# Kernel optimization log

Measured on AMD Instinct MI355X. Metric: run time of the kernel, lower is better.

Reference implementation:

```python
import jax, jax.numpy as jnp
import numpy as np

IN_DIM, HID, MEM, OUT = 512, 1024, 1024, 512
BATCH = 4096
HIST = 5  # hist_steps hard-coded in MMU.__init__

_LINEARS = [("inpgate", IN_DIM, HID), ("rec_inpgate", OUT, HID), ("mem_inpgate", MEM, HID),
            ("inp", IN_DIM, HID), ("rec_inp", OUT, HID),
            ("readgate", IN_DIM, MEM), ("rec_readgate", OUT, MEM), ("mem_readgate", MEM, MEM),
            ("decoder", HID, MEM),
            ("writegate", IN_DIM, MEM), ("rec_writegate", OUT, MEM), ("mem_writegate", MEM, MEM),
            ("encoder", MEM, HID)]


def setup_inputs() -> dict:
    key = jax.random.key(0)
    ks = iter(jax.random.split(key, 2 * len(_LINEARS) + 4))
    d = {"input": jax.random.normal(next(ks), (IN_DIM, BATCH), jnp.float32)}
    for name, fin, fout in _LINEARS:
        bound = 1.0 / np.sqrt(fin)  # torch nn.Linear default init range
        d["W_" + name] = jax.random.uniform(next(ks), (fout, fin), jnp.float32, -bound, bound)
        d["b_" + name] = jax.random.uniform(next(ks), (fout,), jnp.float32, -bound, bound)
    d["w_hid_out"] = jax.random.uniform(next(ks), (OUT, MEM), jnp.float32)  # torch.rand
    return d


def reference(input, W_inpgate, b_inpgate, W_rec_inpgate, b_rec_inpgate,
              W_mem_inpgate, b_mem_inpgate, W_inp, b_inp, W_rec_inp, b_rec_inp,
              W_readgate, b_readgate, W_rec_readgate, b_rec_readgate,
              W_mem_readgate, b_mem_readgate, W_decoder, b_decoder,
              W_writegate, b_writegate, W_rec_writegate, b_rec_writegate,
              W_mem_writegate, b_mem_writegate, W_encoder, b_encoder, w_hid_out):
    B = input.shape[1]
    lin = lambda x, W, b: x @ W.T + b
    # fresh module: history is zeros except last slot = current input (transposed to [B, in])
    xs = jnp.concatenate([jnp.zeros((HIST - 1, B, IN_DIM), input.dtype), input.T[None]], axis=0)

    def step(carry, x):
        out, mem = carry  # [B, OUT], [B, MEM]
        block_inp = jax.nn.sigmoid(lin(x, W_inp, b_inp) + lin(out, W_rec_inp, b_rec_inp))
        inp_gate = jax.nn.sigmoid(lin(x, W_inpgate, b_inpgate) + lin(mem, W_mem_inpgate, b_mem_inpgate)
                                  + lin(out, W_rec_inpgate, b_rec_inpgate))
        read_gate = jax.nn.sigmoid(lin(x, W_readgate, b_readgate) + lin(mem, W_mem_readgate, b_mem_readgate)
                                   + lin(out, W_rec_readgate, b_rec_readgate))
        decoded_mem = lin(read_gate * mem, W_decoder, b_decoder)
        hidden = decoded_mem + block_inp * inp_gate  # [B, HID] (HID == MEM)
        write_gate = jax.nn.sigmoid(lin(x, W_writegate, b_writegate) + lin(mem, W_mem_writegate, b_mem_writegate)
                                    + lin(out, W_rec_writegate, b_rec_writegate))
        encoded = jnp.tanh(lin(hidden, W_encoder, b_encoder))
        mem = (1.0 - write_gate) * mem + write_gate * encoded
        out = hidden @ w_hid_out.T  # w_hid_out.mm(hidden.T).T
        return (out, mem), None

    init = (jnp.zeros((B, OUT), input.dtype), jnp.zeros((B, MEM), input.dtype))
    (out, _mem), _ = jax.lax.scan(step, init, xs)
    return out
```

## Files before the change

### kernel.cpp

```cpp
#include <hip/hip_runtime.h>
#include <hip/hip_bf16.h>
#include <math.h>

typedef __hip_bfloat16 bf16;
typedef __attribute__((ext_vector_type(8))) short s16x8;
typedef __attribute__((ext_vector_type(4))) float f32x4;

__device__ __forceinline__ float fsig(float x) {
  return __builtin_amdgcn_rcpf(1.0f + __expf(-x));
}
__device__ __forceinline__ float ftanh(float x) { return 2.0f * fsig(2.0f * x) - 1.0f; }
__device__ __forceinline__ float dot4(float4 a, float4 b) {
  return a.x * b.x + a.y * b.y + a.z * b.z + a.w * b.w;
}
__device__ __forceinline__ float wred(float s) {
#pragma unroll
  for (int off = 32; off > 0; off >>= 1) s += __shfl_down(s, off, 64);
  return s;
}
__device__ __forceinline__ float b2f(unsigned short u) {
  return __uint_as_float((unsigned)u << 16);
}
__device__ __forceinline__ float4 b2f4(ushort4 u) {
  return make_float4(b2f(u.x), b2f(u.y), b2f(u.z), b2f(u.w));
}

#define WG7_STRIDE 5120

__global__ void setup(const float* __restrict__ W_inp, const float* __restrict__ W_ig,
                      const float* __restrict__ W_rg, const float* __restrict__ W_ho,
                      const float* __restrict__ W_dec, const float* __restrict__ W_enc,
                      const float* __restrict__ input,
                      const float* __restrict__ Wri, const float* __restrict__ Wmig,
                      const float* __restrict__ Wrig, const float* __restrict__ Wmrg,
                      const float* __restrict__ Wrrg, const float* __restrict__ Wmwg,
                      const float* __restrict__ Wrwg,
                      const float* __restrict__ b_inp, const float* __restrict__ b_rinp,
                      const float* __restrict__ b_ig, const float* __restrict__ b_mig,
                      const float* __restrict__ b_rig, const float* __restrict__ b_wg,
                      const float* __restrict__ b_mwg, const float* __restrict__ b_rwg,
                      const float* __restrict__ b_dec, const float* __restrict__ b_enc,
                      bf16* __restrict__ Wcat,
                      bf16* __restrict__ WhoB, bf16* __restrict__ Wcat2, bf16* __restrict__ Wdt,
                      bf16* __restrict__ WencB, bf16* __restrict__ Xb,
                      float* __restrict__ out_s, float* __restrict__ mem_s,
                      float* __restrict__ vout, float* __restrict__ Web,
                      bf16* __restrict__ Wg7) {
  __shared__ float t[32][33];
  const int id = blockIdx.x, tid = threadIdx.x;
  if (id < 12288) {
    const int i = id * 256 + tid;
    if (i < 524288) {
      Wcat[i] = __float2bfloat16(W_inp[i]);
    } else if (i < 1048576) {
      Wcat[i] = __float2bfloat16(W_ig[i - 524288]);
    } else if (i < 1572864) {
      Wcat[i] = __float2bfloat16(W_rg[i - 1048576]);
    } else if (i < 2097152) {
      const int k = i - 1572864;
      const bf16 vv = __float2bfloat16(W_ho[k]);
      WhoB[k] = vv;
      Wcat2[(size_t)(k >> 10) * 2048 + (k & 1023)] = vv;
    } else {
      const int k = i - 2097152;
      WencB[k] = __float2bfloat16(W_enc[k]);
    }
  } else if (id < 14336) {
    const int b = id - 12288;
    const int i0 = (b >> 7) * 32, b0 = (b & 127) * 32;
    const int tx = tid & 31, ty = tid >> 5;
#pragma unroll
    for (int r = ty; r < 32; r += 8) t[r][tx] = input[(size_t)(i0 + r) * 4096 + b0 + tx];
    __syncthreads();
#pragma unroll
    for (int r = ty; r < 32; r += 8)
      Xb[(size_t)(b0 + r) * 512 + i0 + tx] = __float2bfloat16(t[tx][r]);
  } else if (id < 15360) {
    const int b = id - 14336;
    const int j0 = (b >> 5) * 32, k0 = (b & 31) * 32;
    const int tx = tid & 31, ty = tid >> 5;
#pragma unroll
    for (int r = ty; r < 32; r += 8) t[r][tx] = W_dec[(size_t)(j0 + r) * 1024 + k0 + tx];
    __syncthreads();
#pragma unroll
    for (int r = ty; r < 32; r += 8)
      Wdt[(size_t)(k0 + r) * 1024 + j0 + tx] = __float2bfloat16(t[tx][r]);
  } else if (id < 16896) {
    const int o = id - 15360;
    const float* row = (o < 512) ? (W_ho + (size_t)o * 1024) : (W_enc + (size_t)(o - 512) * 1024);
    const float4 a = *(const float4*)(row + tid * 4);
    const float4 b = *(const float4*)(b_dec + tid * 4);
    float s = wred(dot4(a, b));
    if ((tid & 63) == 0) t[0][tid >> 6] = s;
    __syncthreads();
    if (tid == 0) {
      const float d = t[0][0] + t[0][1] + t[0][2] + t[0][3];
      if (o < 512) vout[o] = d;
      else Web[o - 512] = d;
    }
  } else if (id < 18432) {
    const int id2 = id - 16896;
    const float4 bd = *(const float4*)(b_dec + tid * 4);
    const float4 v1 = *(const float4*)(b_inp + tid * 4);
    const float4 v2 = *(const float4*)(b_rinp + tid * 4);
    const float4 v3 = *(const float4*)(b_ig + tid * 4);
    const float4 v4 = *(const float4*)(b_mig + tid * 4);
    const float4 v5 = *(const float4*)(b_rig + tid * 4);
    float4 hv;
    hv.x = bd.x + fsig(v1.x + v2.x) * fsig(v3.x + v4.x + v5.x);
    hv.y = bd.y + fsig(v1.y + v2.y) * fsig(v3.y + v4.y + v5.y);
    hv.z = bd.z + fsig(v1.z + v2.z) * fsig(v3.z + v4.z + v5.z);
    hv.w = bd.w + fsig(v1.w + v2.w) * fsig(v3.w + v4.w + v5.w);
    const float* row =
        (id2 < 1024) ? (W_enc + (size_t)id2 * 1024) : (W_ho + (size_t)(id2 - 1024) * 1024);
    float s = wred(dot4(*(const float4*)(row + tid * 4), hv));
    if ((tid & 63) == 0) t[0][tid >> 6] = s;
    __syncthreads();
    if (tid == 0) {
      const float d = t[0][0] + t[0][1] + t[0][2] + t[0][3];
      if (id2 < 1024) {
        const float wg = fsig(b_wg[id2] + b_mwg[id2] + b_rwg[id2]);
        mem_s[id2] = wg * ftanh(b_enc[id2] + d);
      } else {
        out_s[id2 - 1024] = d;
      }
    }
  } else {
    const int b = id - 18432;
    const int j = b / 5, f = b - j * 5;
    const int col = f * 1024 + tid * 4;
    const float* src;
    int c0, stride;
    if (col < 512)       { src = Wri;  c0 = col;        stride = 512; }
    else if (col < 1536) { src = Wmig; c0 = col - 512;  stride = 1024; }
    else if (col < 2048) { src = Wrig; c0 = col - 1536; stride = 512; }
    else if (col < 3072) { src = Wmrg; c0 = col - 2048; stride = 1024; }
    else if (col < 3584) { src = Wrrg; c0 = col - 3072; stride = 512; }
    else if (col < 4608) { src = Wmwg; c0 = col - 3584; stride = 1024; }
    else                 { src = Wrwg; c0 = col - 4608; stride = 512; }
    const float4 v = *(const float4*)(src + (size_t)j * stride + c0);
    ushort4 u;
    u.x = __bfloat16_as_ushort(__float2bfloat16(v.x));
    u.y = __bfloat16_as_ushort(__float2bfloat16(v.y));
    u.z = __bfloat16_as_ushort(__float2bfloat16(v.z));
    u.w = __bfloat16_as_ushort(__float2bfloat16(v.w));
    *(ushort4*)(Wg7 + (size_t)j * WG7_STRIDE + col) = u;
  }
}

__global__ __launch_bounds__(256) void gates_pe(
    const bf16* __restrict__ Wg7, const float* __restrict__ b_inp,
    const float* __restrict__ b_rinp, const float* __restrict__ b_ig,
    const float* __restrict__ b_mig, const float* __restrict__ b_rig,
    const float* __restrict__ b_rg, const float* __restrict__ b_mrg,
    const float* __restrict__ b_rrg, const float* __restrict__ b_wg,
    const float* __restrict__ b_mwg, const float* __restrict__ b_rwg,
    const float* __restrict__ out_s, const float* __restrict__ mem_s,
    float* __restrict__ rgm, float* __restrict__ h0v, float* __restrict__ wgv,
    const bf16* __restrict__ WhoB, const bf16* __restrict__ WencB,
    const bf16* __restrict__ Wdt, bf16* __restrict__ Pb, bf16* __restrict__ Eb,
    int pe_blocks) {
  __shared__ char smem[32768];
  const int tid = threadIdx.x;
  if ((int)blockIdx.x >= pe_blocks) {
    float(*red)[4] = (float(*)[4])smem;
    const int j = blockIdx.x - pe_blocks, lane = tid & 63, wave = tid >> 6;
    const float4 z = make_float4(0.f, 0.f, 0.f, 0.f);
    const float4 o4 = (tid < 128) ? *(const float4*)(out_s + tid * 4) : z;
    const float4 m4 = *(const float4*)(mem_s + tid * 4);
    const bf16* rowb = Wg7 + (size_t)j * WG7_STRIDE;
    float p[7];
    p[0] = (tid < 128) ? dot4(b2f4(*(const ushort4*)(rowb + tid * 4)), o4) : 0.f;
    p[1] = dot4(b2f4(*(const ushort4*)(rowb + 512 + tid * 4)), m4);
    p[2] = (tid < 128) ? dot4(b2f4(*(const ushort4*)(rowb + 1536 + tid * 4)), o4) : 0.f;
    p[3] = dot4(b2f4(*(const ushort4*)(rowb + 2048 + tid * 4)), m4);
    p[4] = (tid < 128) ? dot4(b2f4(*(const ushort4*)(rowb + 3072 + tid * 4)), o4) : 0.f;
    p[5] = dot4(b2f4(*(const ushort4*)(rowb + 3584 + tid * 4)), m4);
    p[6] = (tid < 128) ? dot4(b2f4(*(const ushort4*)(rowb + 4608 + tid * 4)), o4) : 0.f;
#pragma unroll
    for (int d = 0; d < 7; ++d) {
      float s = wred(p[d]);
      if (lane == 0) red[d][wave] = s;
    }
    __syncthreads();
    if (tid == 0) {
      float D[7];
#pragma unroll
      for (int d = 0; d < 7; ++d) D[d] = red[d][0] + red[d][1] + red[d][2] + red[d][3];
      const float abi = b_inp[j] + b_rinp[j] + D[0];
      const float aig = b_ig[j] + b_mig[j] + b_rig[j] + D[1] + D[2];
      const float arg = b_rg[j] + b_mrg[j] + b_rrg[j] + D[3] + D[4];
      const float awg = b_wg[j] + b_mwg[j] + b_rwg[j] + D[5] + D[6];
      rgm[j] = fsig(arg) * mem_s[j];
      h0v[j] = fsig(abi) * fsig(aig);
      wgv[j] = fsig(awg);
    }
    return;
  }
  const int bi = blockIdx.x;
  const bf16* Ag;
  bf16* Cg;
  int m0, n0;
  if (bi < 128) {
    Ag = WhoB; Cg = Pb;
    m0 = (bi >> 4) * 64; n0 = (bi & 15) * 64;
  } else {
    const int b2 = bi - 128;
    Ag = WencB; Cg = Eb;
    m0 = (b2 >> 4) * 64; n0 = (b2 & 15) * 64;
  }
  const int wave = tid >> 6, lane = tid & 63;
  const int wm = wave >> 1, wn = wave & 1;
  f32x4 acc[2][2] = {};

  auto STAGE = [&](int kt, unsigned bofs) {
#pragma unroll
    for (int i = 0; i < 2; ++i) {
      const int ci = i * 256 + tid;
      const int row = ci >> 3, ck = (ci & 7) ^ (row & 7);
      const bf16* g = Ag + (size_t)(m0 + row) * 1024 + kt + ck * 8;
      const unsigned lofs =
          (unsigned)__builtin_amdgcn_readfirstlane(bofs + (i * 256 + wave * 64) * 16);
      __builtin_amdgcn_global_load_lds(
          (const __attribute__((address_space(1))) void*)g,
          (__attribute__((address_space(3))) void*)(smem + lofs), 16, 0, 0);
    }
#pragma unroll
    for (int i = 0; i < 2; ++i) {
      const int ci = i * 256 + tid;
      const int row = ci >> 3, ck = (ci & 7) ^ (row & 7);
      const bf16* g = Wdt + (size_t)(n0 + row) * 1024 + kt + ck * 8;
      const unsigned lofs =
          (unsigned)__builtin_amdgcn_readfirstlane(bofs + 8192 + (i * 256 + wave * 64) * 16);
      __builtin_amdgcn_global_load_lds(
          (const __attribute__((address_space(1))) void*)g,
          (__attribute__((address_space(3))) void*)(smem + lofs), 16, 0, 0);
    }
  };

  STAGE(0, 0);
  __syncthreads();
  unsigned cur = 0;
  for (int kt = 0; kt < 1024; kt += 64) {
    if (kt + 64 < 1024) STAGE(kt + 64, (cur ^ 1u) * 16384u);
#pragma unroll
    for (int ks = 0; ks < 2; ++ks) {
      const int ckk = ks * 4 + (lane >> 4);
      const unsigned cofs = cur * 16384u;
      s16x8 af[2];
#pragma unroll
      for (int i = 0; i < 2; ++i) {
        const int R = wm * 32 + i * 16 + (lane & 15);
        af[i] = *(const s16x8*)(smem + cofs + (R * 8 + (ckk ^ (R & 7))) * 16);
      }
#pragma unroll
      for (int j = 0; j < 2; ++j) {
        const int R = wn * 32 + j * 16 + (lane & 15);
        const s16x8 bfr = *(const s16x8*)(smem + cofs + 8192 + (R * 8 + (ckk ^ (R & 7))) * 16);
#pragma unroll
        for (int i = 0; i < 2; ++i)
          acc[i][j] = __builtin_amdgcn_mfma_f32_16x16x32_bf16(af[i], bfr, acc[i][j], 0, 0, 0);
      }
    }
    __syncthreads();
    cur ^= 1u;
  }
  const int mb = (lane >> 4) * 4, nb = lane & 15;
#pragma unroll
  for (int i = 0; i < 2; ++i) {
#pragma unroll
    for (int j = 0; j < 2; ++j) {
      const int col = n0 + wn * 32 + j * 16 + nb;
#pragma unroll
      for (int r = 0; r < 4; ++r) {
        const int rowg = m0 + wm * 32 + i * 16 + mb + r;
        Cg[(size_t)rowg * 1024 + col] = __float2bfloat16(acc[i][j][r]);
      }
    }
  }
}

__global__ void step_fuse(const bf16* __restrict__ Eb, const bf16* __restrict__ WencB,
                          const bf16* __restrict__ Pb, const bf16* __restrict__ WhoB,
                          const float* __restrict__ b_enc, const float* __restrict__ Web,
                          const float* __restrict__ vout, const float* __restrict__ rgm,
                          const float* __restrict__ h0v, const float* __restrict__ wgv,
                          float* __restrict__ mem_s, float* __restrict__ out_s) {
  __shared__ float red[4];
  const int id = blockIdx.x, tid = threadIdx.x;
  const float4 r4 = *(const float4*)(rgm + tid * 4);
  const float4 h4 = *(const float4*)(h0v + tid * 4);
  const bf16* Ar = (id < 1024) ? (Eb + (size_t)id * 1024) : (Pb + (size_t)(id - 1024) * 1024);
  const bf16* Br =
      (id < 1024) ? (WencB + (size_t)id * 1024) : (WhoB + (size_t)(id - 1024) * 1024);
  const float4 a4 = b2f4(*(const ushort4*)(Ar + tid * 4));
  const float4 b4 = b2f4(*(const ushort4*)(Br + tid * 4));
  const float s = wred(dot4(a4, r4) + dot4(b4, h4));
  if ((tid & 63) == 0) red[tid >> 6] = s;
  __syncthreads();
  if (tid == 0) {
    const float d = red[0] + red[1] + red[2] + red[3];
    if (id < 1024) {
      const float wg = wgv[id];
      mem_s[id] = (1.0f - wg) * mem_s[id] + wg * ftanh(b_enc[id] + Web[id] + d);
    } else {
      out_s[id - 1024] = vout[id - 1024] + d;
    }
  }
}

__global__ void final_consts(const bf16* __restrict__ Wg7, const float* __restrict__ b_inp,
                             const float* __restrict__ b_rinp, const float* __restrict__ b_ig,
                             const float* __restrict__ b_mig, const float* __restrict__ b_rig,
                             const float* __restrict__ b_rg, const float* __restrict__ b_mrg,
                             const float* __restrict__ b_rrg, const float* __restrict__ out_s,
                             const float* __restrict__ mem_s, const bf16* __restrict__ Pb,
                             float* __restrict__ ccat, bf16* __restrict__ Wcat2) {
  __shared__ float red[5][4];
  const int id = blockIdx.x, tid = threadIdx.x, lane = tid & 63, wave = tid >> 6;
  if (id < 1024) {
    const float4 z = make_float4(0.f, 0.f, 0.f, 0.f);
    const float4 o4 = (tid < 128) ? *(const float4*)(out_s + tid * 4) : z;
    const float4 m4 = *(const float4*)(mem_s + tid * 4);
    const bf16* rowb = Wg7 + (size_t)id * WG7_STRIDE;
    float p[5];
    p[0] = (tid < 128) ? dot4(b2f4(*(const ushort4*)(rowb + tid * 4)), o4) : 0.f;
    p[1] = dot4(b2f4(*(const ushort4*)(rowb + 512 + tid * 4)), m4);
    p[2] = (tid < 128) ? dot4(b2f4(*(const ushort4*)(rowb + 1536 + tid * 4)), o4) : 0.f;
    p[3] = dot4(b2f4(*(const ushort4*)(rowb + 2048 + tid * 4)), m4);
    p[4] = (tid < 128) ? dot4(b2f4(*(const ushort4*)(rowb + 3072 + tid * 4)), o4) : 0.f;
#pragma unroll
    for (int d = 0; d < 5; ++d) {
      float s = wred(p[d]);
      if (lane == 0) red[d][wave] = s;
    }
    __syncthreads();
    if (tid == 0) {
      float D[5];
#pragma unroll
      for (int d = 0; d < 5; ++d) D[d] = red[d][0] + red[d][1] + red[d][2] + red[d][3];
      ccat[id] = b_inp[id] + b_rinp[id] + D[0];
      ccat[1024 + id] = b_ig[id] + b_mig[id] + b_rig[id] + D[1] + D[2];
      ccat[2048 + id] = b_rg[id] + b_mrg[id] + b_rrg[id] + D[3] + D[4];
    }
  } else {
    const int idx = (id - 1024) * 256 + tid;
    const int k = idx & 1023;
    const float pv = b2f(((const unsigned short*)Pb)[idx]);
    Wcat2[(size_t)(idx >> 10) * 2048 + 1024 + k] = __float2bfloat16(pv * mem_s[k]);
  }
}

__global__ __launch_bounds__(256, 4) void gemm_gates(const bf16* __restrict__ A,
                                                     const bf16* __restrict__ Wcat,
                                                     const float* __restrict__ ccat,
                                                     bf16* __restrict__ Hcat) {
  __shared__ char smem[32768];
  const int tid = threadIdx.x, wave = tid >> 6, lane = tid & 63;
  const int wm = wave >> 1, wn = wave & 1;
  const int swz = (blockIdx.x & 7) * 128 + (blockIdx.x >> 3);
  const int m0 = (swz >> 4) * 64, n0 = (swz & 15) * 64;
  f32x4 acc[3][2][2] = {};

  for (int kt = 0; kt < 512; kt += 64) {
    __syncthreads();
#pragma unroll
    for (int i = 0; i < 2; ++i) {
      const int ci = i * 256 + tid;
      const int row = ci >> 3, ck = (ci & 7) ^ (row & 7);
      const bf16* g = A + (size_t)(m0 + row) * 512 + kt + ck * 8;
      const unsigned lofs = (unsigned)__builtin_amdgcn_readfirstlane((i * 256 + wave * 64) * 16);
      __builtin_amdgcn_global_load_lds(
          (const __attribute__((address_space(1))) void*)g,
          (__attribute__((address_space(3))) void*)(smem + lofs), 16, 0, 0);
    }
#pragma unroll
    for (int gI = 0; gI < 3; ++gI) {
      const bf16* Bp = Wcat + gI * 524288;
#pragma unroll
      for (int i = 0; i < 2; ++i) {
        const int ci = i * 256 + tid;
        const int row = ci >> 3, ck = (ci & 7) ^ (row & 7);
        const bf16* g = Bp + (size_t)(n0 + row) * 512 + kt + ck * 8;
        const unsigned lofs = (unsigned)__builtin_amdgcn_readfirstlane(
            8192 + gI * 8192 + (i * 256 + wave * 64) * 16);
        __builtin_amdgcn_global_load_lds(
            (const __attribute__((address_space(1))) void*)g,
            (__attribute__((address_space(3))) void*)(smem + lofs), 16, 0, 0);
      }
    }
    __syncthreads();

#pragma unroll
    for (int ks = 0; ks < 2; ++ks) {
      const int ckk = ks * 4 + (lane >> 4);
      s16x8 af[2];
#pragma unroll
      for (int i = 0; i < 2; ++i) {
        const int R = wm * 32 + i * 16 + (lane & 15);
        af[i] = *(const s16x8*)(smem + (R * 8 + (ckk ^ (R & 7))) * 16);
      }
#pragma unroll
      for (int gI = 0; gI < 3; ++gI) {
#pragma unroll
        for (int j = 0; j < 2; ++j) {
          const int R = wn * 32 + j * 16 + (lane & 15);
          const s16x8 bfr =
              *(const s16x8*)(smem + 8192 + gI * 8192 + (R * 8 + (ckk ^ (R & 7))) * 16);
#pragma unroll
          for (int i = 0; i < 2; ++i)
            acc[gI][i][j] =
                __builtin_amdgcn_mfma_f32_16x16x32_bf16(af[i], bfr, acc[gI][i][j], 0, 0, 0);
        }
      }
    }
  }

  __syncthreads();
  bf16* sm = (bf16*)smem;
  bf16* sr = (bf16*)smem + 5120;
  const int mb = (lane >> 4) * 4, nb = lane & 15;
#pragma unroll
  for (int i = 0; i < 2; ++i) {
#pragma unroll
    for (int j = 0; j < 2; ++j) {
      const int colL = wn * 32 + j * 16 + nb;
      const int jg = n0 + colL;
      const float c0 = ccat[jg], c1 = ccat[1024 + jg], c2 = ccat[2048 + jg];
#pragma unroll
      for (int r = 0; r < 4; ++r) {
        const int rowL = wm * 32 + i * 16 + mb + r;
        const float h = fsig(acc[0][i][j][r] + c0) * fsig(acc[1][i][j][r] + c1);
        const float rg = fsig(acc[2][i][j][r] + c2);
        sm[rowL * 80 + colL] = __float2bfloat16(h);
        sr[rowL * 80 + colL] = __float2bfloat16(rg);
      }
    }
  }
  __syncthreads();
#pragma unroll
  for (int pp = 0; pp < 2; ++pp) {
    const int c = pp * 256 + tid;
    const int row = c >> 3, cc = c & 7;
    const s16x8 v0 = *(const s16x8*)(sm + row * 80 + cc * 8);
    const s16x8 v1 = *(const s16x8*)(sr + row * 80 + cc * 8);
    *(s16x8*)(Hcat + (size_t)(m0 + row) * 2048 + n0 + cc * 8) = v0;
    *(s16x8*)(Hcat + (size_t)(m0 + row) * 2048 + 1024 + n0 + cc * 8) = v1;
  }
}

__global__ __launch_bounds__(256, 4) void gemm_out(const bf16* __restrict__ A,
                                                   const bf16* __restrict__ Bp,
                                                   const float* __restrict__ vout,
                                                   float* __restrict__ outF) {
  __shared__ char smem[32768];
  const int tid = threadIdx.x, wave = tid >> 6, lane = tid & 63;
  const int wm = wave >> 1, wn = wave & 1;
  const int swz = (blockIdx.x & 7) * 64 + (blockIdx.x >> 3);
  const int m0 = (swz >> 3) * 64, n0 = (swz & 7) * 64;
  f32x4 acc[2][2] = {};

  auto STAGE = [&](int kt, unsigned bofs) {
#pragma unroll
    for (int i = 0; i < 2; ++i) {
      const int ci = i * 256 + tid;
      const int row = ci >> 3, ck = (ci & 7) ^ (row & 7);
      const bf16* g = A + (size_t)(m0 + row) * 2048 + kt + ck * 8;
      const unsigned lofs =
          (unsigned)__builtin_amdgcn_readfirstlane(bofs + (i * 256 + wave * 64) * 16);
      __builtin_amdgcn_global_load_lds(
          (const __attribute__((address_space(1))) void*)g,
          (__attribute__((address_space(3))) void*)(smem + lofs), 16, 0, 0);
    }
#pragma unroll
    for (int i = 0; i < 2; ++i) {
      const int ci = i * 256 + tid;
      const int row = ci >> 3, ck = (ci & 7) ^ (row & 7);
      const bf16* g = Bp + (size_t)(n0 + row) * 2048 + kt + ck * 8;
      const unsigned lofs =
          (unsigned)__builtin_amdgcn_readfirstlane(bofs + 8192 + (i * 256 + wave * 64) * 16);
      __builtin_amdgcn_global_load_lds(
          (const __attribute__((address_space(1))) void*)g,
          (__attribute__((address_space(3))) void*)(smem + lofs), 16, 0, 0);
    }
  };

  STAGE(0, 0);
  __syncthreads();
  unsigned cur = 0;
  for (int kt = 0; kt < 2048; kt += 64) {
    if (kt + 64 < 2048) STAGE(kt + 64, (cur ^ 1u) * 16384u);
#pragma unroll
    for (int ks = 0; ks < 2; ++ks) {
      const int ckk = ks * 4 + (lane >> 4);
      const unsigned cofs = cur * 16384u;
      s16x8 af[2];
#pragma unroll
      for (int i = 0; i < 2; ++i) {
        const int R = wm * 32 + i * 16 + (lane & 15);
        af[i] = *(const s16x8*)(smem + cofs + (R * 8 + (ckk ^ (R & 7))) * 16);
      }
#pragma unroll
      for (int j = 0; j < 2; ++j) {
        const int R = wn * 32 + j * 16 + (lane & 15);
        const s16x8 bfr = *(const s16x8*)(smem + cofs + 8192 + (R * 8 + (ckk ^ (R & 7))) * 16);
#pragma unroll
        for (int i = 0; i < 2; ++i)
          acc[i][j] = __builtin_amdgcn_mfma_f32_16x16x32_bf16(af[i], bfr, acc[i][j], 0, 0, 0);
      }
    }
    __syncthreads();
    cur ^= 1u;
  }

  const int mb = (lane >> 4) * 4, nb = lane & 15;
#pragma unroll
  for (int i = 0; i < 2; ++i) {
#pragma unroll
    for (int j = 0; j < 2; ++j) {
      const int col = n0 + wn * 32 + j * 16 + nb;
#pragma unroll
      for (int r = 0; r < 4; ++r) {
        const int rowg = m0 + wm * 32 + i * 16 + mb + r;
        outF[(size_t)rowg * 512 + col] = acc[i][j][r] + vout[col];
      }
    }
  }
}

extern "C" void kernel_launch(void* const* d_in, const int* in_sizes, int n_in, void* d_out,
                              int out_size, void* d_ws, size_t ws_size, hipStream_t stream) {
  const float* input  = (const float*)d_in[0];
  const float* W_ig   = (const float*)d_in[1];  const float* b_ig   = (const float*)d_in[2];
  const float* W_rig  = (const float*)d_in[3];  const float* b_rig  = (const float*)d_in[4];
  const float* W_mig  = (const float*)d_in[5];  const float* b_mig  = (const float*)d_in[6];
  const float* W_inp  = (const float*)d_in[7];  const float* b_inp  = (const float*)d_in[8];
  const float* W_rinp = (const float*)d_in[9];  const float* b_rinp = (const float*)d_in[10];
  const float* W_rg   = (const float*)d_in[11]; const float* b_rg   = (const float*)d_in[12];
  const float* W_rrg  = (const float*)d_in[13]; const float* b_rrg  = (const float*)d_in[14];
  const float* W_mrg  = (const float*)d_in[15]; const float* b_mrg  = (const float*)d_in[16];
  const float* W_dec  = (const float*)d_in[17]; const float* b_dec  = (const float*)d_in[18];
  const float* W_wg   = (const float*)d_in[19]; const float* b_wg   = (const float*)d_in[20];
  const float* W_rwg  = (const float*)d_in[21]; const float* b_rwg  = (const float*)d_in[22];
  const float* W_mwg  = (const float*)d_in[23]; const float* b_mwg  = (const float*)d_in[24];
  const float* W_enc  = (const float*)d_in[25]; const float* b_enc  = (const float*)d_in[26];
  const float* W_ho   = (const float*)d_in[27];
  (void)W_wg;

  char* ws = (char*)d_ws;
  float* out_s = (float*)(ws + 0);
  float* mem_s = (float*)(ws + 4096);
  float* rgm   = (float*)(ws + 8192);
  float* h0v   = (float*)(ws + 12288);
  float* wgv   = (float*)(ws + 16384);
  float* ccat  = (float*)(ws + 24576);
  float* vout  = (float*)(ws + 40960);
  float* Web   = (float*)(ws + 45056);
  bf16* Pb     = (bf16*)(ws + 65536);
  bf16* Xb     = (bf16*)(ws + 2162688);
  bf16* Wcat   = (bf16*)(ws + 6356992);
  bf16* WhoB   = (bf16*)(ws + 9502720);
  bf16* Wcat2  = (bf16*)(ws + 10551296);
  bf16* Wdt    = (bf16*)(ws + 12648448);
  bf16* Hcat   = (bf16*)(ws + 14745600);
  bf16* Eb     = (bf16*)(ws + 31522816);
  bf16* WencB  = (bf16*)(ws + 35717120);
  bf16* Wg7    = (bf16*)(ws + 37814272);

  setup<<<23552, 256, 0, stream>>>(W_inp, W_ig, W_rg, W_ho, W_dec, W_enc, input,
                                   W_rinp, W_mig, W_rig, W_mrg, W_rrg, W_mwg, W_rwg,
                                   b_inp, b_rinp, b_ig, b_mig, b_rig, b_wg, b_mwg, b_rwg,
                                   b_dec, b_enc, Wcat, WhoB, Wcat2, Wdt, WencB, Xb,
                                   out_s, mem_s, vout, Web, Wg7);

  for (int s = 0; s < 3; ++s) {
    const int pe = (s == 0) ? 384 : 0;
    gates_pe<<<1024 + pe, 256, 0, stream>>>(Wg7, b_inp, b_rinp, b_ig, b_mig, b_rig, b_rg, b_mrg,
                                            b_rrg, b_wg, b_mwg, b_rwg, out_s, mem_s, rgm, h0v,
                                            wgv, WhoB, WencB, Wdt, Pb, Eb, pe);
    step_fuse<<<1536, 256, 0, stream>>>(Eb, WencB, Pb, WhoB, b_enc, Web, vout, rgm, h0v, wgv,
                                        mem_s, out_s);
  }

  final_consts<<<3072, 256, 0, stream>>>(Wg7, b_inp, b_rinp, b_ig, b_mig, b_rig, b_rg, b_mrg,
                                         b_rrg, out_s, mem_s, Pb, ccat, Wcat2);

  gemm_gates<<<1024, 256, 0, stream>>>(Xb, Wcat, ccat, Hcat);

  gemm_out<<<512, 256, 0, stream>>>(Hcat, Wcat2, vout, (float*)d_out);
}
```

Measured before the change: 218.0 us.

## Double-buffer gate GEMM LDS tiles with smaller K step to overlap loads

Changes the gate GEMM main loop from single-buffered K=64 tiles with two barriers per step to double-buffered K=32 tiles inside the same 32KB of LDS. The next tile is loaded directly into LDS while MFMAs run on the current buffer, with one barrier per iteration. The aim is to hide global-to-LDS load latency behind compute. In exchange, the loop takes twice as many iterations with less work per barrier. There is also a possible hazard: the loop waits only on a barrier, with no explicit vmcnt wait before consuming the async global_load_lds data.

```diff
diff --git a/kernel.cpp b/kernel.cpp
--- a/kernel.cpp
+++ b/kernel.cpp
@@ -362,51 +362,47 @@
   const int m0 = (swz >> 4) * 64, n0 = (swz & 15) * 64;
   f32x4 acc[3][2][2] = {};
 
-  for (int kt = 0; kt < 512; kt += 64) {
-    __syncthreads();
-#pragma unroll
-    for (int i = 0; i < 2; ++i) {
-      const int ci = i * 256 + tid;
-      const int row = ci >> 3, ck = (ci & 7) ^ (row & 7);
+  auto STAGE = [&](int kt, unsigned bofs) {
+    const int row = tid >> 2, ck = (tid & 3) ^ (row & 3);
+    {
       const bf16* g = A + (size_t)(m0 + row) * 512 + kt + ck * 8;
-      const unsigned lofs = (unsigned)__builtin_amdgcn_readfirstlane((i * 256 + wave * 64) * 16);
+      const unsigned lofs = (unsigned)__builtin_amdgcn_readfirstlane(bofs + wave * 1024u);
       __builtin_amdgcn_global_load_lds(
           (const __attribute__((address_space(1))) void*)g,
           (__attribute__((address_space(3))) void*)(smem + lofs), 16, 0, 0);
     }
 #pragma unroll
     for (int gI = 0; gI < 3; ++gI) {
-      const bf16* Bp = Wcat + gI * 524288;
-#pragma unroll
-      for (int i = 0; i < 2; ++i) {
-        const int ci = i * 256 + tid;
-        const int row = ci >> 3, ck = (ci & 7) ^ (row & 7);
-        const bf16* g = Bp + (size_t)(n0 + row) * 512 + kt + ck * 8;
-        const unsigned lofs = (unsigned)__builtin_amdgcn_readfirstlane(
-            8192 + gI * 8192 + (i * 256 + wave * 64) * 16);
-        __builtin_amdgcn_global_load_lds(
-            (const __attribute__((address_space(1))) void*)g,
-            (__attribute__((address_space(3))) void*)(smem + lofs), 16, 0, 0);
-      }
-    }
-    __syncthreads();
-
-#pragma unroll
-    for (int ks = 0; ks < 2; ++ks) {
-      const int ckk = ks * 4 + (lane >> 4);
+      const bf16* g = Wcat + gI * 524288 + (size_t)(n0 + row) * 512 + kt + ck * 8;
+      const unsigned lofs = (unsigned)__builtin_amdgcn_readfirstlane(
+          bofs + 4096u + gI * 4096u + wave * 1024u);
+      __builtin_amdgcn_global_load_lds(
+          (const __attribute__((address_space(1))) void*)g,
+          (__attribute__((address_space(3))) void*)(smem + lofs), 16, 0, 0);
+    }
+  };
+
+  STAGE(0, 0);
+  __syncthreads();
+  unsigned cur = 0;
+  for (int kt = 0; kt < 512; kt += 32) {
+    if (kt + 32 < 512) STAGE(kt + 32, (cur ^ 1u) * 16384u);
+    {
+      const int ckk = lane >> 4;
+      const unsigned cofs = cur * 16384u;
       s16x8 af[2];
 #pragma unroll
       for (int i = 0; i < 2; ++i) {
         const int R = wm * 32 + i * 16 + (lane & 15);
-        af[i] = *(const s16x8*)(smem + (R * 8 + (ckk ^ (R & 7))) * 16);
+        af[i] = *(const s16x8*)(smem + cofs + R * 64 + ((ckk ^ (R & 3)) * 16));
       }
 #pragma unroll
       for (int gI = 0; gI < 3; ++gI) {
 #pragma unroll
         for (int j = 0; j < 2; ++j) {
           const int R = wn * 32 + j * 16 + (lane & 15);
-          const s16x8 bfr =
-              *(const s16x8*)(smem + 8192 + gI * 8192 + (R * 8 + (ckk ^ (R & 7))) * 16);
+          const s16x8 bfr = *(const s16x8*)(smem + cofs + 4096 + gI * 4096 + R * 64 +
+                                            ((ckk ^ (R & 3)) * 16));
 #pragma unroll
           for (int i = 0; i < 2; ++i)
             acc[gI][i][j] =
@@ -414,9 +410,10 @@
         }
       }
     }
-  }
-
-  __syncthreads();
+    __syncthreads();
+    cur ^= 1u;
+  }
+
   bf16* sm = (bf16*)smem;
   bf16* sr = (bf16*)smem + 5120;
   const int mb = (lane >> 4) * 4, nb = lane & 15;
```

New measurement: 219.1 us. Within noise of the previous version (+0.5%).
